# Kernel tuning notes

Measured on AMD Instinct MI355X. Metric: run time of the kernel, lower is better.

## Reference

```python
import jax, jax.numpy as jnp
import numpy as np

B, S, H, NH, HD = 2, 2048, 4096, 32, 128
NEG = jnp.finfo(jnp.float32).min


def rotate_half(x):
    x1, x2 = x[..., : x.shape[-1] // 2], x[..., x.shape[-1] // 2 :]
    return jnp.concatenate((-x2, x1), axis=-1)


def setup_inputs() -> dict:
    key = jax.random.key(0)
    ks = jax.random.split(key, 7)
    return {
        "hidden_states": jax.random.normal(ks[0], (B, S, H), jnp.float32),
        "cos": jax.random.uniform(ks[1], (1, 1, S, HD), jnp.float32),
        "sin": jax.random.uniform(ks[2], (1, 1, S, HD), jnp.float32),
        "Wq": jax.random.normal(ks[3], (H, H), jnp.float32) * 0.02,
        "Wk": jax.random.normal(ks[4], (HD, H), jnp.float32) * 0.02,
        "Wv": jax.random.normal(ks[5], (HD, H), jnp.float32) * 0.02,
        "Wd": jax.random.normal(ks[6], (H, H), jnp.float32) * 0.02,
    }


def reference(hidden_states, cos, sin, Wq, Wk, Wv, Wd):
    b, s, _ = hidden_states.shape
    q = (hidden_states @ Wq.T).reshape(b, s, NH, HD).transpose(0, 2, 1, 3)  # [B,NH,S,HD]
    k = (hidden_states @ Wk.T)[:, None, :, :]  # [B,1,S,HD] (multi-query)
    v = (hidden_states @ Wv.T)[:, None, :, :]
    # inline RoPE
    q = q * cos + rotate_half(q) * sin
    k = k * cos + rotate_half(k) * sin
    scale = 1.0 / jnp.sqrt(jnp.float32(HD))
    scores = jnp.einsum("bhqd,bhkd->bhqk", q, k) * scale
    # causal mask: additive finfo.min above diagonal
    causal = jnp.tril(jnp.ones((s, s), jnp.bool_))
    scores = scores + jnp.where(causal, 0.0, NEG)
    attn = jax.nn.softmax(scores, axis=-1)
    out = jnp.einsum("bhqk,bhkd->bhqd", attn, v)  # [B,NH,S,HD]
    out = out.transpose(0, 2, 1, 3).reshape(b, s, NH * HD)
    return out @ Wd.T
```

## Files before the change

### kernel.cpp

```cpp
#include <hip/hip_runtime.h>
#include <hip/hip_bf16.h>

constexpr int Bc  = 2;
constexpr int Sc  = 2048;
constexpr int Hc  = 4096;
constexpr int NHc = 32;
constexpr int HDc = 128;

typedef __attribute__((ext_vector_type(8))) __bf16 bf16x8;
typedef __attribute__((ext_vector_type(4))) __bf16 bf16x4;
typedef __attribute__((ext_vector_type(4))) float  f32x4;

#if defined(__has_builtin)
#if __has_builtin(__builtin_amdgcn_global_load_lds)
#define HAS_GLL 1
#endif
#endif
#ifndef HAS_GLL
#define HAS_GLL 0
#endif

__device__ __forceinline__ void gll16(const __bf16* g, __bf16* lds_base, int lane) {
#if HAS_GLL
    __builtin_amdgcn_global_load_lds((const __attribute__((address_space(1))) void*)g,
                                     (__attribute__((address_space(3))) void*)lds_base,
                                     16, 0, 0);
#else
    *(int4*)(lds_base + lane * 8) = *(const int4*)g;
#endif
}

__global__ void cvt_f32_bf16(const float* __restrict__ in, __bf16* __restrict__ out, int n) {
    int i = (blockIdx.x * blockDim.x + threadIdx.x) * 4;
    if (i >= n) return;
    const float4 v = *(const float4*)(in + i);
    bf16x4 o;
    o[0] = (__bf16)v.x; o[1] = (__bf16)v.y; o[2] = (__bf16)v.z; o[3] = (__bf16)v.w;
    *(bf16x4*)(out + i) = o;
}

__global__ void build_wkv(const float* __restrict__ Wk, const float* __restrict__ Wv,
                          __bf16* __restrict__ out) {
    int i = (blockIdx.x * blockDim.x + threadIdx.x) * 4;
    if (i >= 256 * Hc) return;
    int row = i >> 12;
    int col = i & (Hc - 1);
    const float* src = (row < HDc) ? (Wk + (long)row * Hc + col)
                                   : (Wv + (long)(row - HDc) * Hc + col);
    const float4 v = *(const float4*)src;
    bf16x4 o;
    o[0] = (__bf16)v.x; o[1] = (__bf16)v.y; o[2] = (__bf16)v.z; o[3] = (__bf16)v.w;
    *(bf16x4*)(out + i) = o;
}

template <typename OUT>
__global__ __launch_bounds__(256)
void gemm_bt(const __bf16* __restrict__ A, const __bf16* __restrict__ B,
             OUT* __restrict__ C, int M, int N, int K) {
    __shared__ __bf16 As[128][64];
    __shared__ __bf16 Bs[128][64];

    const int tid  = threadIdx.x;
    const int wave = tid >> 6, lane = tid & 63;
    const int lrow = lane & 15, quad = lane >> 4;
    const int m0   = blockIdx.y * 128;
    const int n0   = blockIdx.x * 128;
    const int wr   = (wave >> 1) * 64;
    const int wc   = (wave & 1) * 64;

    f32x4 acc[4][4] = {};

    int srow[4], scol[4];
#pragma unroll
    for (int it = 0; it < 4; ++it) {
        int e = (wave * 4 + it) * 1024 + lane * 16;
        int r = e >> 7;
        int cb = (e >> 4) & 7;
        srow[it] = r;
        scol[it] = ((cb ^ (r & 7)) * 8);
    }
    const __bf16* Ab = A + (long)m0 * K;
    const __bf16* Bb = B + (long)n0 * K;

    const int fcol0 = ((quad ^ (lrow & 7)) << 3);
    const int fcol1 = (((4 | quad) ^ (lrow & 7)) << 3);

    const int nk = K >> 6;
    for (int kt = 0; kt < nk; ++kt) {
        const long k0 = (long)kt * 64;
        __syncthreads();
#pragma unroll
        for (int it = 0; it < 4; ++it)
            gll16(Ab + (long)srow[it] * K + k0 + scol[it], &As[0][0] + (wave * 4 + it) * 512, lane);
#pragma unroll
        for (int it = 0; it < 4; ++it)
            gll16(Bb + (long)srow[it] * K + k0 + scol[it], &Bs[0][0] + (wave * 4 + it) * 512, lane);
        __syncthreads();

#pragma unroll
        for (int c = 0; c < 2; ++c) {
            const int fc = c ? fcol1 : fcol0;
            bf16x8 af[4], bfv[4];
#pragma unroll
            for (int i = 0; i < 4; ++i) af[i]  = *(const bf16x8*)&As[wr + i * 16 + lrow][fc];
#pragma unroll
            for (int j = 0; j < 4; ++j) bfv[j] = *(const bf16x8*)&Bs[wc + j * 16 + lrow][fc];
#pragma unroll
            for (int i = 0; i < 4; ++i)
#pragma unroll
                for (int j = 0; j < 4; ++j)
                    acc[i][j] = __builtin_amdgcn_mfma_f32_16x16x32_bf16(af[i], bfv[j], acc[i][j], 0, 0, 0);
        }
    }

#pragma unroll
    for (int i = 0; i < 4; ++i) {
        const int row = m0 + wr + i * 16 + quad * 4;
#pragma unroll
        for (int j = 0; j < 4; ++j) {
            const int col = n0 + wc + j * 16 + lrow;
            OUT* cp = C + (long)row * N + col;
#pragma unroll
            for (int r = 0; r < 4; ++r) cp[(long)r * N] = (OUT)acc[i][j][r];
        }
    }
}

template <typename OUT>
__global__ __launch_bounds__(256)
void gemm_bt64(const __bf16* __restrict__ A, const __bf16* __restrict__ B,
               OUT* __restrict__ C, int M, int N, int K) {
    __shared__ __bf16 As[64][64];
    __shared__ __bf16 Bs[64][64];

    const int tid  = threadIdx.x;
    const int wave = tid >> 6, lane = tid & 63;
    const int lrow = lane & 15, quad = lane >> 4;
    const int m0   = blockIdx.y * 64;
    const int n0   = blockIdx.x * 64;
    const int wr   = (wave >> 1) * 32;
    const int wc   = (wave & 1) * 32;

    f32x4 acc[2][2] = {};

    int srow[2], scol[2];
#pragma unroll
    for (int it = 0; it < 2; ++it) {
        int e = (wave * 2 + it) * 1024 + lane * 16;
        int r = e >> 7;
        int cb = (e >> 4) & 7;
        srow[it] = r;
        scol[it] = ((cb ^ (r & 7)) * 8);
    }
    const __bf16* Ab = A + (long)m0 * K;
    const __bf16* Bb = B + (long)n0 * K;

    const int fcol0 = ((quad ^ (lrow & 7)) << 3);
    const int fcol1 = (((4 | quad) ^ (lrow & 7)) << 3);

    const int nk = K >> 6;
    for (int kt = 0; kt < nk; ++kt) {
        const long k0 = (long)kt * 64;
        __syncthreads();
#pragma unroll
        for (int it = 0; it < 2; ++it)
            gll16(Ab + (long)srow[it] * K + k0 + scol[it], &As[0][0] + (wave * 2 + it) * 512, lane);
#pragma unroll
        for (int it = 0; it < 2; ++it)
            gll16(Bb + (long)srow[it] * K + k0 + scol[it], &Bs[0][0] + (wave * 2 + it) * 512, lane);
        __syncthreads();

#pragma unroll
        for (int c = 0; c < 2; ++c) {
            const int fc = c ? fcol1 : fcol0;
            bf16x8 af[2], bfv[2];
#pragma unroll
            for (int i = 0; i < 2; ++i) af[i]  = *(const bf16x8*)&As[wr + i * 16 + lrow][fc];
#pragma unroll
            for (int j = 0; j < 2; ++j) bfv[j] = *(const bf16x8*)&Bs[wc + j * 16 + lrow][fc];
#pragma unroll
            for (int i = 0; i < 2; ++i)
#pragma unroll
                for (int j = 0; j < 2; ++j)
                    acc[i][j] = __builtin_amdgcn_mfma_f32_16x16x32_bf16(af[i], bfv[j], acc[i][j], 0, 0, 0);
        }
    }

#pragma unroll
    for (int i = 0; i < 2; ++i) {
        const int row = m0 + wr + i * 16 + quad * 4;
#pragma unroll
        for (int j = 0; j < 2; ++j) {
            const int col = n0 + wc + j * 16 + lrow;
            OUT* cp = C + (long)row * N + col;
#pragma unroll
            for (int r = 0; r < 4; ++r) cp[(long)r * N] = (OUT)acc[i][j][r];
        }
    }
}

__global__ void rope_q(__bf16* __restrict__ Q, const float* __restrict__ cosb,
                       const float* __restrict__ sinb, float scale) {
    int gid  = blockIdx.x * blockDim.x + threadIdx.x;
    int row  = gid >> 8;
    int rem  = gid & 255;
    int h    = rem >> 3;
    int dblk = (rem & 7) * 8;
    int s    = row & (Sc - 1);
    __bf16* p = Q + (long)row * Hc + h * HDc;
    const float* cp = cosb + s * HDc;
    const float* sp = sinb + s * HDc;
    bf16x8 lo = *(bf16x8*)(p + dblk);
    bf16x8 hi = *(bf16x8*)(p + dblk + 64);
    bf16x8 olo, ohi;
#pragma unroll
    for (int j = 0; j < 8; ++j) {
        float ql = (float)lo[j], qh = (float)hi[j];
        float cl = cp[dblk + j],      sl = sp[dblk + j];
        float ch = cp[dblk + 64 + j], sh = sp[dblk + 64 + j];
        olo[j] = (__bf16)((ql * cl - qh * sl) * scale);
        ohi[j] = (__bf16)((qh * ch + ql * sh) * scale);
    }
    *(bf16x8*)(p + dblk)      = olo;
    *(bf16x8*)(p + dblk + 64) = ohi;
}

__global__ void rope_k(__bf16* __restrict__ KV, const float* __restrict__ cosb,
                       const float* __restrict__ sinb) {
    int gid  = blockIdx.x * blockDim.x + threadIdx.x;
    int row  = gid >> 3;
    int dblk = (gid & 7) * 8;
    int s    = row & (Sc - 1);
    __bf16* p = KV + (long)row * 256;
    const float* cp = cosb + s * HDc;
    const float* sp = sinb + s * HDc;
    bf16x8 lo = *(bf16x8*)(p + dblk);
    bf16x8 hi = *(bf16x8*)(p + dblk + 64);
    bf16x8 olo, ohi;
#pragma unroll
    for (int j = 0; j < 8; ++j) {
        float ql = (float)lo[j], qh = (float)hi[j];
        float cl = cp[dblk + j],      sl = sp[dblk + j];
        float ch = cp[dblk + 64 + j], sh = sp[dblk + 64 + j];
        olo[j] = (__bf16)(ql * cl - qh * sl);
        ohi[j] = (__bf16)(qh * ch + ql * sh);
    }
    *(bf16x8*)(p + dblk)      = olo;
    *(bf16x8*)(p + dblk + 64) = ohi;
}

__global__ void vtrans(const __bf16* __restrict__ KV, __bf16* __restrict__ Vt) {
    __shared__ __bf16 T[128][72];
    const int tid = threadIdx.x;
    const int s0  = (blockIdx.x & (Sc / 64 - 1)) * 64;
    const int b   = blockIdx.x / (Sc / 64);
#pragma unroll
    for (int i = 0; i < 4; ++i) {
        int e = i * 256 + tid;
        int s = e >> 4, dc = (e & 15) * 8;
        bf16x8 v = *(const bf16x8*)(KV + (long)(b * Sc + s0 + s) * 256 + 128 + dc);
#pragma unroll
        for (int j = 0; j < 8; ++j) T[dc + j][s] = v[j];
    }
    __syncthreads();
#pragma unroll
    for (int i = 0; i < 4; ++i) {
        int e = i * 256 + tid;
        int d = e >> 3, sc8 = (e & 7) * 8;
        bf16x8 v;
#pragma unroll
        for (int j = 0; j < 8; ++j) v[j] = T[d][sc8 + j];
        *(bf16x8*)(Vt + (long)(b * HDc + d) * Sc + s0 + sc8) = v;
    }
}

__global__ __launch_bounds__(256, 2)
void attn(const __bf16* __restrict__ Q,
          const __bf16* __restrict__ KV,
          const __bf16* __restrict__ Vt,
          __bf16* __restrict__ O) {
    const int qt   = (gridDim.x - 1) - blockIdx.x;
    const int bh   = blockIdx.y;
    const int b    = bh >> 5, h = bh & 31;
    const int tid  = threadIdx.x;
    const int wave = tid >> 6, lane = tid & 63;
    const int lrow = lane & 15, quad = lane >> 4;

    __shared__ __bf16 Ks[2][64][128];
    __shared__ __bf16 Vs[2][128][64];
    __shared__ __bf16 Vones[16][72];
    __shared__ __bf16 Ps[4][16][72];

    for (int idx = tid; idx < 16 * 72; idx += 256)
        Vones[idx / 72][idx % 72] = (__bf16)1.0f;

    const int q0 = qt * 128 + wave * 32;

    bf16x8 aq[2][4];
#pragma unroll
    for (int qq = 0; qq < 2; ++qq) {
        const __bf16* qp = Q + (long)(b * Sc + q0 + qq * 16 + lrow) * Hc + h * HDc + quad * 8;
#pragma unroll
        for (int c = 0; c < 4; ++c) aq[qq][c] = *(const bf16x8*)(qp + c * 32);
    }

    f32x4 o[2][8] = {};
    f32x4 lac[2] = {};
    float mst[2][4];
#pragma unroll
    for (int qq = 0; qq < 2; ++qq)
#pragma unroll
        for (int r = 0; r < 4; ++r) mst[qq][r] = -3.0e38f;

    const __bf16* kvb = KV + (long)b * Sc * 256;
    const __bf16* vtb = Vt + (long)b * HDc * Sc;
    int krow[4], kcol[4], vrow[4], vcol[4];
#pragma unroll
    for (int it = 0; it < 4; ++it) {
        int e = (wave * 4 + it) * 1024 + lane * 16;
        int rk = e >> 8, cbk = (e >> 4) & 15;
        krow[it] = rk; kcol[it] = ((cbk ^ (rk & 15)) * 8);
        int rv = e >> 7, cbv = (e >> 4) & 7;
        vrow[it] = rv; vcol[it] = ((cbv ^ (rv & 7)) * 8);
    }

    auto stage = [&](int kt, int bu) {
#pragma unroll
        for (int it = 0; it < 4; ++it) {
            gll16(kvb + (long)(kt * 64 + krow[it]) * 256 + kcol[it],
                  &Ks[bu][0][0] + (wave * 4 + it) * 512, lane);
            gll16(vtb + (long)vrow[it] * Sc + kt * 64 + vcol[it],
                  &Vs[bu][0][0] + (wave * 4 + it) * 512, lane);
        }
    };

    const int nt = 2 * qt + 2;
    stage(0, 0);

    for (int kt = 0; kt < nt; ++kt) {
        __syncthreads();
        if (kt + 1 < nt) stage(kt + 1, (kt + 1) & 1);
        const int bu = kt & 1;

        f32x4 sc[2][4] = {};
        __builtin_amdgcn_s_setprio(1);
#pragma unroll
        for (int ct = 0; ct < 4; ++ct) {
#pragma unroll
            for (int c = 0; c < 4; ++c) {
                bf16x8 bk = *(const bf16x8*)&Ks[bu][ct * 16 + lrow][(((c << 2) | quad) ^ lrow) << 3];
                sc[0][ct] = __builtin_amdgcn_mfma_f32_16x16x32_bf16(aq[0][c], bk, sc[0][ct], 0, 0, 0);
                sc[1][ct] = __builtin_amdgcn_mfma_f32_16x16x32_bf16(aq[1][c], bk, sc[1][ct], 0, 0, 0);
            }
        }
        __builtin_amdgcn_s_setprio(0);

        bf16x8 ap[2][2];
#pragma unroll
        for (int qq = 0; qq < 2; ++qq) {
            if (kt * 64 + 63 > q0 + qq * 16) {
#pragma unroll
                for (int ct = 0; ct < 4; ++ct) {
                    int kv = kt * 64 + ct * 16 + lrow;
#pragma unroll
                    for (int r = 0; r < 4; ++r) {
                        int qr = q0 + qq * 16 + quad * 4 + r;
                        if (kv > qr) sc[qq][ct][r] = -3.0e38f;
                    }
                }
            }

            float lmax[4];
#pragma unroll
            for (int r = 0; r < 4; ++r)
                lmax[r] = fmaxf(fmaxf(sc[qq][0][r], sc[qq][1][r]),
                                fmaxf(sc[qq][2][r], sc[qq][3][r]));
            const bool near_ok = (lmax[0] <= mst[qq][0] + 8.0f) &&
                                 (lmax[1] <= mst[qq][1] + 8.0f) &&
                                 (lmax[2] <= mst[qq][2] + 8.0f) &&
                                 (lmax[3] <= mst[qq][3] + 8.0f);
            if (!__all(near_ok)) {
                float alf[4];
#pragma unroll
                for (int r = 0; r < 4; ++r) {
                    float mx = lmax[r];
#pragma unroll
                    for (int off = 1; off < 16; off <<= 1) mx = fmaxf(mx, __shfl_xor(mx, off, 64));
                    float mnew = fmaxf(mst[qq][r], mx);
                    alf[r]     = __expf(mst[qq][r] - mnew);
                    mst[qq][r] = mnew;
                }
#pragma unroll
                for (int dt = 0; dt < 8; ++dt)
#pragma unroll
                    for (int r = 0; r < 4; ++r) o[qq][dt][r] *= alf[r];
#pragma unroll
                for (int r = 0; r < 4; ++r) lac[qq][r] *= alf[r];
            }
#pragma unroll
            for (int ct = 0; ct < 4; ++ct)
#pragma unroll
                for (int r = 0; r < 4; ++r)
                    sc[qq][ct][r] = __expf(sc[qq][ct][r] - mst[qq][r]);

#pragma unroll
            for (int ct = 0; ct < 4; ++ct)
#pragma unroll
                for (int r = 0; r < 4; ++r)
                    Ps[wave][quad * 4 + r][ct * 16 + lrow] = (__bf16)sc[qq][ct][r];
#pragma unroll
            for (int ks = 0; ks < 2; ++ks)
                ap[qq][ks] = *(const bf16x8*)&Ps[wave][lrow][ks * 32 + quad * 8];
        }

        __builtin_amdgcn_s_setprio(1);
#pragma unroll
        for (int dt = 0; dt < 8; ++dt) {
#pragma unroll
            for (int ks = 0; ks < 2; ++ks) {
                bf16x8 bv = *(const bf16x8*)&Vs[bu][dt * 16 + lrow]
                                [(((ks << 2) | quad) ^ (lrow & 7)) << 3];
#pragma unroll
                for (int qq = 0; qq < 2; ++qq)
                    o[qq][dt] = __builtin_amdgcn_mfma_f32_16x16x32_bf16(ap[qq][ks], bv, o[qq][dt], 0, 0, 0);
            }
        }
#pragma unroll
        for (int ks = 0; ks < 2; ++ks) {
            bf16x8 bv = *(const bf16x8*)&Vones[lrow][ks * 32 + quad * 8];
#pragma unroll
            for (int qq = 0; qq < 2; ++qq)
                lac[qq] = __builtin_amdgcn_mfma_f32_16x16x32_bf16(ap[qq][ks], bv, lac[qq], 0, 0, 0);
        }
        __builtin_amdgcn_s_setprio(0);
    }

#pragma unroll
    for (int qq = 0; qq < 2; ++qq)
#pragma unroll
        for (int r = 0; r < 4; ++r) {
            float inv = 1.f / lac[qq][r];
            int qr = q0 + qq * 16 + quad * 4 + r;
            __bf16* op = O + (long)(b * Sc + qr) * Hc + h * HDc;
#pragma unroll
            for (int dt = 0; dt < 8; ++dt) op[dt * 16 + lrow] = (__bf16)(o[qq][dt][r] * inv);
        }
}

extern "C" void kernel_launch(void* const* d_in, const int* in_sizes, int n_in,
                              void* d_out, int out_size, void* d_ws, size_t ws_size,
                              hipStream_t stream) {
    const float* hs   = (const float*)d_in[0];
    const float* cosb = (const float*)d_in[1];
    const float* sinb = (const float*)d_in[2];
    const float* Wq   = (const float*)d_in[3];
    const float* Wk   = (const float*)d_in[4];
    const float* Wv   = (const float*)d_in[5];
    const float* Wd   = (const float*)d_in[6];
    float* out = (float*)d_out;

    char* ws = (char*)d_ws;
    const long SZ_HS  = (long)Bc * Sc * Hc * 2;
    const long SZ_W   = (long)Hc * Hc * 2;
    const long SZ_KV  = (long)Bc * Sc * 256 * 2;
    __bf16* hs16  = (__bf16*)(ws);
    __bf16* wq16  = (__bf16*)(ws + SZ_HS);
    __bf16* wkv16 = (__bf16*)(ws + SZ_HS + SZ_W);
    __bf16* q16   = (__bf16*)(ws + SZ_HS + SZ_W + SZ_KV);
    __bf16* kv16  = (__bf16*)(ws + SZ_HS + SZ_W + SZ_KV + SZ_HS);
    __bf16* vt16  = (__bf16*)(ws + SZ_HS + SZ_W + SZ_KV + SZ_HS + SZ_KV);
    __bf16* att16 = hs16;
    __bf16* wd16  = wq16;

    const int nHS = Bc * Sc * Hc;
    const int nW  = Hc * Hc;

    cvt_f32_bf16<<<nHS / 1024, 256, 0, stream>>>(hs, hs16, nHS);
    cvt_f32_bf16<<<nW / 1024, 256, 0, stream>>>(Wq, wq16, nW);
    build_wkv<<<(256 * Hc) / 1024, 256, 0, stream>>>(Wk, Wv, wkv16);

    gemm_bt<__bf16><<<dim3(Hc / 128, (Bc * Sc) / 128), 256, 0, stream>>>(
        hs16, wq16, q16, Bc * Sc, Hc, Hc);
    gemm_bt64<__bf16><<<dim3(256 / 64, (Bc * Sc) / 64), 256, 0, stream>>>(
        hs16, wkv16, kv16, Bc * Sc, 256, Hc);

    cvt_f32_bf16<<<nW / 1024, 256, 0, stream>>>(Wd, wd16, nW);

    const float scale = 0.08838834764831845f;
    rope_q<<<(Bc * Sc * NHc * 8) / 256, 256, 0, stream>>>(q16, cosb, sinb, scale);
    rope_k<<<(Bc * Sc * 8) / 256, 256, 0, stream>>>(kv16, cosb, sinb);
    vtrans<<<Bc * (Sc / 64), 256, 0, stream>>>(kv16, vt16);

    attn<<<dim3(Sc / 128, Bc * NHc), 256, 0, stream>>>(q16, kv16, vt16, att16);

    gemm_bt<float><<<dim3(Hc / 128, (Bc * Sc) / 128), 256, 0, stream>>>(
        att16, wd16, out, Bc * Sc, Hc, Hc);
}
```

Before: 799.6 us.

## Use double-buffered 256x256 GEMM with XCD swizzle; exp2 softmax in attention

Replaces the 128x128 single-buffered projection GEMM with a 512-thread 256x256 tile kernel. It double-buffers LDS and splits each k-step into four quarter stages, each with a global-to-LDS prefetch, a vmcnt wait, barriers and raised MFMA priority. It also remaps block IDs so neighbouring tiles land on the same XCD. In attention, log2(e) is folded into the Q scale so exp2f replaces __expf, and the ones vector for the row-sum MFMA moves from LDS to a register. The larger tiles increase reuse and hide load latency, at the cost of more LDS and registers per block, lower occupancy and more barriers per k-step.

```diff
diff --git a/kernel.cpp b/kernel.cpp
--- a/kernel.cpp
+++ b/kernel.cpp
@@ -1,5 +1,6 @@
 #include <hip/hip_runtime.h>
 #include <hip/hip_bf16.h>
+#include <math.h>
 
 constexpr int Bc  = 2;
 constexpr int Sc  = 2048;
@@ -19,6 +20,10 @@
 #ifndef HAS_GLL
 #define HAS_GLL 0
 #endif
+
+#define CFENCE asm volatile("" ::: "memory")
+#define BARRIER do { CFENCE; __builtin_amdgcn_s_barrier(); CFENCE; } while (0)
+#define WAITVM(n) asm volatile("s_waitcnt vmcnt(" #n ")" ::: "memory")
 
 __device__ __forceinline__ void gll16(const __bf16* g, __bf16* lds_base, int lane) {
 #if HAS_GLL
@@ -54,71 +59,148 @@
 }
 
 template <typename OUT>
-__global__ __launch_bounds__(256)
-void gemm_bt(const __bf16* __restrict__ A, const __bf16* __restrict__ B,
+__global__ __launch_bounds__(512, 2)
+void gemm256(const __bf16* __restrict__ A, const __bf16* __restrict__ B,
              OUT* __restrict__ C, int M, int N, int K) {
-    __shared__ __bf16 As[128][64];
-    __shared__ __bf16 Bs[128][64];
+    __shared__ __bf16 As[2][256 * 64];
+    __shared__ __bf16 Bs[2][256 * 64];
 
     const int tid  = threadIdx.x;
     const int wave = tid >> 6, lane = tid & 63;
     const int lrow = lane & 15, quad = lane >> 4;
-    const int m0   = blockIdx.y * 128;
-    const int n0   = blockIdx.x * 128;
-    const int wr   = (wave >> 1) * 64;
-    const int wc   = (wave & 1) * 64;
-
-    f32x4 acc[4][4] = {};
-
-    int srow[4], scol[4];
-#pragma unroll
-    for (int it = 0; it < 4; ++it) {
-        int e = (wave * 4 + it) * 1024 + lane * 16;
-        int r = e >> 7;
-        int cb = (e >> 4) & 7;
-        srow[it] = r;
-        scol[it] = ((cb ^ (r & 7)) * 8);
+    const int wm = wave >> 2, wn = wave & 3;
+
+    const int nwg = gridDim.x * gridDim.y;
+    const int bid = blockIdx.y * gridDim.x + blockIdx.x;
+    const int wg  = (bid & 7) * (nwg >> 3) + (bid >> 3);
+    const int m0  = (wg / gridDim.x) * 256;
+    const int n0  = (wg % gridDim.x) * 256;
+
+    f32x4 acc[8][4] = {};
+
+    int srow[4][2], sbase[4][2];
+    const int rp   = lane >> 3;
+    const int scol = ((lane & 7) ^ rp) << 3;
+#pragma unroll
+    for (int it = 0; it < 2; ++it) {
+        const int c   = wave * 2 + it;
+        const int rb0 = (c < 8) ? c * 8 : 128 + (c - 8) * 8;
+        const int rb1 = (c >> 2) * 64 + (c & 3) * 8;
+        srow[0][it] = rb0 + rp;       sbase[0][it] = rb0 * 64;
+        srow[1][it] = rb1 + rp;       sbase[1][it] = rb1 * 64;
+        srow[2][it] = rb1 + 32 + rp;  sbase[2][it] = (rb1 + 32) * 64;
+        srow[3][it] = rb0 + 64 + rp;  sbase[3][it] = (rb0 + 64) * 64;
     }
     const __bf16* Ab = A + (long)m0 * K;
     const __bf16* Bb = B + (long)n0 * K;
 
-    const int fcol0 = ((quad ^ (lrow & 7)) << 3);
-    const int fcol1 = (((4 | quad) ^ (lrow & 7)) << 3);
+    auto stageg = [&](int g, int bu, long k0) {
+        const __bf16* gb = (g == 0 || g == 3) ? Ab : Bb;
+        __bf16* lb = (g == 0 || g == 3) ? &As[bu][0] : &Bs[bu][0];
+#pragma unroll
+        for (int it = 0; it < 2; ++it)
+            gll16(gb + (long)srow[g][it] * K + k0 + scol, lb + sbase[g][it], lane);
+    };
+
+    const int fc0  = ((quad ^ (lrow & 7)) << 3);
+    const int fc1  = (((4 | quad) ^ (lrow & 7)) << 3);
+    const int arow = wm * 128 + lrow;
+    const int brow = wn * 64 + lrow;
 
     const int nk = K >> 6;
+    stageg(0, 0, 0); stageg(1, 0, 0); stageg(2, 0, 0); stageg(3, 0, 0);
+    WAITVM(4);
+    BARRIER;
+
     for (int kt = 0; kt < nk; ++kt) {
-        const long k0 = (long)kt * 64;
-        __syncthreads();
-#pragma unroll
-        for (int it = 0; it < 4; ++it)
-            gll16(Ab + (long)srow[it] * K + k0 + scol[it], &As[0][0] + (wave * 4 + it) * 512, lane);
-#pragma unroll
-        for (int it = 0; it < 4; ++it)
-            gll16(Bb + (long)srow[it] * K + k0 + scol[it], &Bs[0][0] + (wave * 4 + it) * 512, lane);
-        __syncthreads();
-
-#pragma unroll
-        for (int c = 0; c < 2; ++c) {
-            const int fc = c ? fcol1 : fcol0;
-            bf16x8 af[4], bfv[4];
-#pragma unroll
-            for (int i = 0; i < 4; ++i) af[i]  = *(const bf16x8*)&As[wr + i * 16 + lrow][fc];
-#pragma unroll
-            for (int j = 0; j < 4; ++j) bfv[j] = *(const bf16x8*)&Bs[wc + j * 16 + lrow][fc];
-#pragma unroll
-            for (int i = 0; i < 4; ++i)
-#pragma unroll
-                for (int j = 0; j < 4; ++j)
-                    acc[i][j] = __builtin_amdgcn_mfma_f32_16x16x32_bf16(af[i], bfv[j], acc[i][j], 0, 0, 0);
-        }
-    }
-
-#pragma unroll
-    for (int i = 0; i < 4; ++i) {
-        const int row = m0 + wr + i * 16 + quad * 4;
+        const int bu = kt & 1;
+        const bool more = (kt + 1 < nk);
+        const long k1 = (long)(kt + 1) * 64;
+        bf16x8 af[2][4], bv0[2][2], bv1[2][2];
+
+#pragma unroll
+        for (int i2 = 0; i2 < 4; ++i2) {
+            af[0][i2] = *(const bf16x8*)&As[bu][(arow + i2 * 16) * 64 + fc0];
+            af[1][i2] = *(const bf16x8*)&As[bu][(arow + i2 * 16) * 64 + fc1];
+        }
+#pragma unroll
+        for (int j2 = 0; j2 < 2; ++j2) {
+            bv0[0][j2] = *(const bf16x8*)&Bs[bu][(brow + j2 * 16) * 64 + fc0];
+            bv0[1][j2] = *(const bf16x8*)&Bs[bu][(brow + j2 * 16) * 64 + fc1];
+        }
+        if (more) { stageg(0, bu ^ 1, k1); WAITVM(4); } else { WAITVM(0); }
+        BARRIER;
+        __builtin_amdgcn_s_setprio(1);
+#pragma unroll
+        for (int c = 0; c < 2; ++c)
+#pragma unroll
+            for (int i2 = 0; i2 < 4; ++i2)
+#pragma unroll
+                for (int j2 = 0; j2 < 2; ++j2)
+                    acc[i2][j2] = __builtin_amdgcn_mfma_f32_16x16x32_bf16(
+                        af[c][i2], bv0[c][j2], acc[i2][j2], 0, 0, 0);
+        __builtin_amdgcn_s_setprio(0);
+        BARRIER;
+
+#pragma unroll
+        for (int j2 = 0; j2 < 2; ++j2) {
+            bv1[0][j2] = *(const bf16x8*)&Bs[bu][(brow + 32 + j2 * 16) * 64 + fc0];
+            bv1[1][j2] = *(const bf16x8*)&Bs[bu][(brow + 32 + j2 * 16) * 64 + fc1];
+        }
+        if (more) { stageg(1, bu ^ 1, k1); WAITVM(4); } else { WAITVM(0); }
+        BARRIER;
+        __builtin_amdgcn_s_setprio(1);
+#pragma unroll
+        for (int c = 0; c < 2; ++c)
+#pragma unroll
+            for (int i2 = 0; i2 < 4; ++i2)
+#pragma unroll
+                for (int j2 = 0; j2 < 2; ++j2)
+                    acc[i2][2 + j2] = __builtin_amdgcn_mfma_f32_16x16x32_bf16(
+                        af[c][i2], bv1[c][j2], acc[i2][2 + j2], 0, 0, 0);
+        __builtin_amdgcn_s_setprio(0);
+        BARRIER;
+
+#pragma unroll
+        for (int i2 = 0; i2 < 4; ++i2) {
+            af[0][i2] = *(const bf16x8*)&As[bu][(arow + 64 + i2 * 16) * 64 + fc0];
+            af[1][i2] = *(const bf16x8*)&As[bu][(arow + 64 + i2 * 16) * 64 + fc1];
+        }
+        if (more) { stageg(2, bu ^ 1, k1); WAITVM(4); } else { WAITVM(0); }
+        BARRIER;
+        __builtin_amdgcn_s_setprio(1);
+#pragma unroll
+        for (int c = 0; c < 2; ++c)
+#pragma unroll
+            for (int i2 = 0; i2 < 4; ++i2)
+#pragma unroll
+                for (int j2 = 0; j2 < 2; ++j2)
+                    acc[4 + i2][j2] = __builtin_amdgcn_mfma_f32_16x16x32_bf16(
+                        af[c][i2], bv0[c][j2], acc[4 + i2][j2], 0, 0, 0);
+        __builtin_amdgcn_s_setprio(0);
+        BARRIER;
+
+        if (more) { stageg(3, bu ^ 1, k1); WAITVM(4); } else { WAITVM(0); }
+        BARRIER;
+        __builtin_amdgcn_s_setprio(1);
+#pragma unroll
+        for (int c = 0; c < 2; ++c)
+#pragma unroll
+            for (int i2 = 0; i2 < 4; ++i2)
+#pragma unroll
+                for (int j2 = 0; j2 < 2; ++j2)
+                    acc[4 + i2][2 + j2] = __builtin_amdgcn_mfma_f32_16x16x32_bf16(
+                        af[c][i2], bv1[c][j2], acc[4 + i2][2 + j2], 0, 0, 0);
+        __builtin_amdgcn_s_setprio(0);
+        BARRIER;
+    }
+
+#pragma unroll
+    for (int i = 0; i < 8; ++i) {
+        const int row = m0 + wm * 128 + i * 16 + quad * 4;
 #pragma unroll
         for (int j = 0; j < 4; ++j) {
-            const int col = n0 + wc + j * 16 + lrow;
+            const int col = n0 + wn * 64 + j * 16 + lrow;
             OUT* cp = C + (long)row * N + col;
 #pragma unroll
             for (int r = 0; r < 4; ++r) cp[(long)r * N] = (OUT)acc[i][j][r];
@@ -288,11 +370,11 @@
 
     __shared__ __bf16 Ks[2][64][128];
     __shared__ __bf16 Vs[2][128][64];
-    __shared__ __bf16 Vones[16][72];
     __shared__ __bf16 Ps[4][16][72];
 
-    for (int idx = tid; idx < 16 * 72; idx += 256)
-        Vones[idx / 72][idx % 72] = (__bf16)1.0f;
+    bf16x8 vone;
+#pragma unroll
+    for (int j = 0; j < 8; ++j) vone[j] = (__bf16)1.0f;
 
     const int q0 = qt * 128 + wave * 32;
 
@@ -387,7 +469,7 @@
 #pragma unroll
                     for (int off = 1; off < 16; off <<= 1) mx = fmaxf(mx, __shfl_xor(mx, off, 64));
                     float mnew = fmaxf(mst[qq][r], mx);
-                    alf[r]     = __expf(mst[qq][r] - mnew);
+                    alf[r]     = exp2f(mst[qq][r] - mnew);
                     mst[qq][r] = mnew;
                 }
 #pragma unroll
@@ -401,7 +483,7 @@
             for (int ct = 0; ct < 4; ++ct)
 #pragma unroll
                 for (int r = 0; r < 4; ++r)
-                    sc[qq][ct][r] = __expf(sc[qq][ct][r] - mst[qq][r]);
+                    sc[qq][ct][r] = exp2f(sc[qq][ct][r] - mst[qq][r]);
 
 #pragma unroll
             for (int ct = 0; ct < 4; ++ct)
@@ -427,10 +509,9 @@
         }
 #pragma unroll
         for (int ks = 0; ks < 2; ++ks) {
-            bf16x8 bv = *(const bf16x8*)&Vones[lrow][ks * 32 + quad * 8];
 #pragma unroll
             for (int qq = 0; qq < 2; ++qq)
-                lac[qq] = __builtin_amdgcn_mfma_f32_16x16x32_bf16(ap[qq][ks], bv, lac[qq], 0, 0, 0);
+                lac[qq] = __builtin_amdgcn_mfma_f32_16x16x32_bf16(ap[qq][ks], vone, lac[qq], 0, 0, 0);
         }
         __builtin_amdgcn_s_setprio(0);
     }
@@ -479,20 +560,20 @@
     cvt_f32_bf16<<<nW / 1024, 256, 0, stream>>>(Wq, wq16, nW);
     build_wkv<<<(256 * Hc) / 1024, 256, 0, stream>>>(Wk, Wv, wkv16);
 
-    gemm_bt<__bf16><<<dim3(Hc / 128, (Bc * Sc) / 128), 256, 0, stream>>>(
+    gemm256<__bf16><<<dim3(Hc / 256, (Bc * Sc) / 256), 512, 0, stream>>>(
         hs16, wq16, q16, Bc * Sc, Hc, Hc);
     gemm_bt64<__bf16><<<dim3(256 / 64, (Bc * Sc) / 64), 256, 0, stream>>>(
         hs16, wkv16, kv16, Bc * Sc, 256, Hc);
 
     cvt_f32_bf16<<<nW / 1024, 256, 0, stream>>>(Wd, wd16, nW);
 
-    const float scale = 0.08838834764831845f;
+    const float scale = 0.08838834764831845f * 1.4426950408889634f;
     rope_q<<<(Bc * Sc * NHc * 8) / 256, 256, 0, stream>>>(q16, cosb, sinb, scale);
     rope_k<<<(Bc * Sc * 8) / 256, 256, 0, stream>>>(kv16, cosb, sinb);
     vtrans<<<Bc * (Sc / 64), 256, 0, stream>>>(kv16, vt16);
 
     attn<<<dim3(Sc / 128, Bc * NHc), 256, 0, stream>>>(q16, kv16, vt16, att16);
 
-    gemm_bt<float><<<dim3(Hc / 128, (Bc * Sc) / 128), 256, 0, stream>>>(
+    gemm256<float><<<dim3(Hc / 256, (Bc * Sc) / 256), 512, 0, stream>>>(
         att16, wd16, out, Bc * Sc, Hc, Hc);
 }
```

Result: faster. 698.8 us (-12.6%).
